# Kernel optimization log

Hardware: AMD Instinct MI355X
Metric: run time of the kernel (lower is better)

Reference implementation:

```python
import jax, jax.numpy as jnp
import numpy as np

N = 50000   # nodes
E = 600000  # edges
D = 128     # embedding_dim
L = 4       # num_message_passing_steps


def setup_inputs() -> dict:
    key = jax.random.key(0)
    ks = jax.random.split(key, 5)
    x = jax.random.normal(ks[0], (N, D), dtype=jnp.float32)
    edge_index = jax.random.randint(ks[1], (2, E), 0, N, dtype=jnp.int32)
    # Per-layer params: MPNN linear (no bias), GCNConv weight + bias.
    lin_w = jax.random.normal(ks[2], (L, D, D), dtype=jnp.float32) / np.sqrt(D).astype(np.float32)
    gcn_w = jax.random.normal(ks[3], (L, D, D), dtype=jnp.float32) / np.sqrt(D).astype(np.float32)
    gcn_b = jax.random.normal(ks[4], (L, D), dtype=jnp.float32) * 0.01
    return {"x": x, "edge_index": edge_index, "lin_w": lin_w, "gcn_w": gcn_w, "gcn_b": gcn_b}


def reference(x, edge_index, lin_w, gcn_w, gcn_b):
    n = x.shape[0]
    # GCNConv defaults: add_self_loops=True, normalize=True.
    loops = jnp.arange(n, dtype=edge_index.dtype)
    src = jnp.concatenate([edge_index[0], loops])  # [E+N]
    dst = jnp.concatenate([edge_index[1], loops])  # [E+N]
    # Degree computed on dst (col) for flow='source_to_target'.
    deg = jax.ops.segment_sum(jnp.ones_like(src, dtype=x.dtype), dst, num_segments=n)
    dinv = jnp.where(deg > 0, jax.lax.rsqrt(jnp.maximum(deg, 1.0)), 0.0)
    norm = dinv[src] * dinv[dst]  # [E+N]

    for l in range(lin_w.shape[0]):
        h = x @ lin_w[l].T                 # MPNNLayer.linear (no bias)
        h = h @ gcn_w[l].T                 # GCNConv internal linear
        msgs = h[src] * norm[:, None]      # gather + normalize  [E+N, D]
        agg = jax.ops.segment_sum(msgs, dst, num_segments=n)
        x = agg + gcn_b[l]                 # GCNConv bias
        # NOTE: self.relu is `Sequential as ReLU` -> empty Sequential = identity.
    return x
```

## Files before the change

kernel.cpp:

```cpp
#include <hip/hip_runtime.h>

#define DEMB 128

typedef __attribute__((ext_vector_type(8))) _Float16 half8;
typedef __attribute__((ext_vector_type(4))) _Float16 half4;
typedef __attribute__((ext_vector_type(4))) float f32x4;

__global__ void kwc(const float* __restrict__ gcn, const float* __restrict__ lin,
                    float* __restrict__ Ms) {
  __shared__ float sa[128];
  int l = blockIdx.x >> 7, i = blockIdx.x & 127, j = threadIdx.x;
  sa[j] = gcn[((size_t)l * 128 + i) * 128 + j];
  __syncthreads();
  float acc = 0.f;
#pragma unroll 8
  for (int k = 0; k < 128; ++k) acc += sa[k] * lin[((size_t)l * 128 + k) * 128 + j];
  Ms[((size_t)l * 128 + i) * 128 + j] = acc;
}

__global__ void ksg(const float* __restrict__ A, const float* __restrict__ B,
                    float* __restrict__ C) {
  __shared__ float sa[128];
  int i = blockIdx.x, j = threadIdx.x;
  sa[j] = A[i * 128 + j];
  __syncthreads();
  float acc = 0.f;
#pragma unroll 8
  for (int k = 0; k < 128; ++k) acc += sa[k] * B[k * 128 + j];
  C[i * 128 + j] = acc;
}

__global__ void ksgh(const float* __restrict__ A, const float* __restrict__ B,
                     _Float16* __restrict__ C) {
  __shared__ float sa[128];
  int i = blockIdx.x, j = threadIdx.x;
  sa[j] = A[i * 128 + j];
  __syncthreads();
  float acc = 0.f;
#pragma unroll 8
  for (int k = 0; k < 128; ++k) acc += sa[k] * B[k * 128 + j];
  C[i * 128 + j] = (_Float16)acc;
}

__global__ void kcvec(const float* __restrict__ Ms, const float* __restrict__ gb,
                      float* __restrict__ cb) {
  __shared__ float t0[128], t1[128];
  int j = threadIdx.x;
  const float* M1 = Ms + 16384;
  const float* M2 = Ms + 2 * 16384;
  const float* M3 = Ms + 3 * 16384;
  float a;
  t0[j] = gb[j]; __syncthreads();
  a = 0.f; for (int k = 0; k < 128; ++k) a += M1[j * 128 + k] * t0[k];
  t1[j] = a; __syncthreads();
  a = 0.f; for (int k = 0; k < 128; ++k) a += M2[j * 128 + k] * t1[k];
  __syncthreads(); t0[j] = a; __syncthreads();
  a = 0.f; for (int k = 0; k < 128; ++k) a += M3[j * 128 + k] * t0[k];
  cb[j] = a;
  __syncthreads(); t0[j] = gb[128 + j]; __syncthreads();
  a = 0.f; for (int k = 0; k < 128; ++k) a += M2[j * 128 + k] * t0[k];
  t1[j] = a; __syncthreads();
  a = 0.f; for (int k = 0; k < 128; ++k) a += M3[j * 128 + k] * t1[k];
  cb[128 + j] = a;
  __syncthreads(); t0[j] = gb[256 + j]; __syncthreads();
  a = 0.f; for (int k = 0; k < 128; ++k) a += M3[j * 128 + k] * t0[k];
  cb[256 + j] = a;
}

__global__ void kinit(int* __restrict__ deg, int* __restrict__ cur, int n) {
  int i = blockIdx.x * 256 + threadIdx.x;
  if (i < n) { deg[i] = 1; cur[i] = 0; }
}

__global__ void kdeg(const int* __restrict__ ei, int* __restrict__ deg, int etot) {
  int i = blockIdx.x * 256 + threadIdx.x;
  if (i < etot) atomicAdd(&deg[ei[etot + i]], 1);
}

__global__ void kscan1(const int* __restrict__ deg, int* __restrict__ off,
                       int* __restrict__ bsum, float* __restrict__ dinv,
                       float* __restrict__ dinv2, int n) {
  __shared__ int s[256];
  int t = threadIdx.x, i = blockIdx.x * 256 + t;
  int c = 0;
  if (i < n) {
    int d = deg[i];
    c = d - 1;
    float dv = rsqrtf((float)d);
    dinv[i] = dv;
    dinv2[i] = dv * dv;
  }
  s[t] = c;
  __syncthreads();
  for (int o = 1; o < 256; o <<= 1) {
    int v = (t >= o) ? s[t - o] : 0;
    __syncthreads();
    s[t] += v;
    __syncthreads();
  }
  if (i < n) off[i] = s[t] - c;
  if (t == 255) bsum[blockIdx.x] = s[t];
}

__global__ void kscan2(const int* __restrict__ bsum, int* __restrict__ boff,
                       int nb, int* __restrict__ off, int n, int etot) {
  __shared__ int s[256];
  int t = threadIdx.x;
  int c = (t < nb) ? bsum[t] : 0;
  s[t] = c;
  __syncthreads();
  for (int o = 1; o < 256; o <<= 1) {
    int v = (t >= o) ? s[t - o] : 0;
    __syncthreads();
    s[t] += v;
    __syncthreads();
  }
  if (t < nb) boff[t] = s[t] - c;
  if (t == 0) off[n] = etot;
}

__global__ void kscan3(int* __restrict__ off, const int* __restrict__ boff, int n) {
  int i = blockIdx.x * 256 + threadIdx.x;
  if (i < n) off[i] += boff[i >> 8];
}

__global__ void kfill(const int* __restrict__ ei, const int* __restrict__ off,
                      int* __restrict__ cur, int* __restrict__ csr, int etot) {
  int i = blockIdx.x * 256 + threadIdx.x;
  if (i < etot) {
    int d = ei[etot + i];
    int p = atomicAdd(&cur[d], 1);
    csr[off[d] + p] = ei[i];
  }
}

__global__ void kspmv(const float* __restrict__ a_in, const float* __restrict__ dinv,
                      const int* __restrict__ csr, const int* __restrict__ off,
                      float* __restrict__ u_out, float* __restrict__ a_out, int n) {
  int i = blockIdx.x * 256 + threadIdx.x;
  if (i >= n) return;
  float s = a_in[i];
  int e = off[i], end = off[i + 1];
  for (; e < end; ++e) s += a_in[csr[e]];
  float u = dinv[i] * s;
  u_out[i] = u;
  a_out[i] = dinv[i] * u;
}

__global__ void kpre(const float* __restrict__ x, const float* __restrict__ dinv,
                     _Float16* __restrict__ xh, int n) {
  int gid = blockIdx.x * 256 + threadIdx.x;
  if (gid >= n * 32) return;
  int r = gid >> 5, c = (gid & 31) * 4;
  float d = dinv[r];
  float4 v = *(const float4*)(x + (size_t)r * DEMB + c);
  half4 o = {(_Float16)(v.x * d), (_Float16)(v.y * d), (_Float16)(v.z * d), (_Float16)(v.w * d)};
  *(half4*)(xh + (size_t)r * DEMB + c) = o;
}

__launch_bounds__(256)
__global__ void kagg16(const _Float16* __restrict__ vin, const int* __restrict__ csr,
                       const int* __restrict__ off, const float* __restrict__ scale,
                       _Float16* __restrict__ vout, int n) {
  int wid = (int)((blockIdx.x * 256u + threadIdx.x) >> 6);
  if (wid >= n) return;
  int lane = threadIdx.x & 63;
  int q = lane >> 4, l16 = lane & 15;
  const _Float16* base = vin + (size_t)8 * l16;
  float acc[8];
  if (q == 0) {
    half8 sv = *(const half8*)(base + (size_t)wid * DEMB);
#pragma unroll
    for (int j = 0; j < 8; ++j) acc[j] = (float)sv[j];
  } else {
#pragma unroll
    for (int j = 0; j < 8; ++j) acc[j] = 0.f;
  }
  int end = off[wid + 1];
  for (int e = off[wid] + 4 * q; e < end; e += 16) {
    int em = end - 1;
    int i0 = csr[e];
    int i1 = csr[min(e + 1, em)];
    int i2 = csr[min(e + 2, em)];
    int i3 = csr[min(e + 3, em)];
    float w1 = (e + 1 < end) ? 1.f : 0.f;
    float w2 = (e + 2 < end) ? 1.f : 0.f;
    float w3 = (e + 3 < end) ? 1.f : 0.f;
    half8 r0 = *(const half8*)(base + (size_t)i0 * DEMB);
    half8 r1 = *(const half8*)(base + (size_t)i1 * DEMB);
    half8 r2 = *(const half8*)(base + (size_t)i2 * DEMB);
    half8 r3 = *(const half8*)(base + (size_t)i3 * DEMB);
#pragma unroll
    for (int j = 0; j < 8; ++j)
      acc[j] += (float)r0[j] + w1 * (float)r1[j] + w2 * (float)r2[j] + w3 * (float)r3[j];
  }
#pragma unroll
  for (int j = 0; j < 8; ++j) {
    acc[j] += __shfl_xor(acc[j], 16);
    acc[j] += __shfl_xor(acc[j], 32);
  }
  if (q == 0) {
    float s = scale[wid];
    half8 o;
#pragma unroll
    for (int j = 0; j < 8; ++j) o[j] = (_Float16)(acc[j] * s);
    *(half8*)(vout + (size_t)wid * DEMB + 8 * l16) = o;
  }
}

__launch_bounds__(256)
__global__ void kgemm16(const _Float16* __restrict__ y, const _Float16* __restrict__ Rh,
                        const float* __restrict__ u1, const float* __restrict__ u2,
                        const float* __restrict__ u3, const float* __restrict__ cb,
                        const float* __restrict__ b3, float* __restrict__ out, int n) {
  int t = threadIdx.x;
  int wv = t >> 6, lane = t & 63;
  int l16 = lane & 15, g = lane >> 4;
  int row0 = blockIdx.x * 128 + wv * 32;
  f32x4 acc[2][8];
#pragma unroll
  for (int w = 0; w < 2; ++w)
#pragma unroll
    for (int n8 = 0; n8 < 8; ++n8) acc[w][n8] = (f32x4){0.f, 0.f, 0.f, 0.f};

#pragma unroll
  for (int k0 = 0; k0 < 128; k0 += 32) {
    half8 a0 = *(const half8*)(y + (size_t)(row0 + l16) * DEMB + k0 + g * 8);
    half8 a1 = *(const half8*)(y + (size_t)(row0 + 16 + l16) * DEMB + k0 + g * 8);
#pragma unroll
    for (int n8 = 0; n8 < 8; ++n8) {
      half8 b = *(const half8*)(Rh + (size_t)(n8 * 16 + l16) * DEMB + k0 + g * 8);
      acc[0][n8] = __builtin_amdgcn_mfma_f32_16x16x32_f16(a0, b, acc[0][n8], 0, 0, 0);
      acc[1][n8] = __builtin_amdgcn_mfma_f32_16x16x32_f16(a1, b, acc[1][n8], 0, 0, 0);
    }
  }
#pragma unroll
  for (int n8 = 0; n8 < 8; ++n8) {
    int col = n8 * 16 + l16;
    float cA = cb[col], cB = cb[128 + col], cC = cb[256 + col], bb = b3[col];
#pragma unroll
    for (int w = 0; w < 2; ++w)
#pragma unroll
      for (int r = 0; r < 4; ++r) {
        int row = row0 + w * 16 + g * 4 + r;
        if (row < n) {
          out[(size_t)row * DEMB + col] =
              acc[w][n8][r] + u3[row] * cA + u2[row] * cB + u1[row] * cC + bb;
        }
      }
  }
}

extern "C" void kernel_launch(void* const* d_in, const int* in_sizes, int n_in,
                              void* d_out, int out_size, void* d_ws, size_t ws_size,
                              hipStream_t stream) {
  const float* x0 = (const float*)d_in[0];
  const int* ei = (const int*)d_in[1];
  const float* lin = (const float*)d_in[2];
  const float* gcn = (const float*)d_in[3];
  const float* gb = (const float*)d_in[4];
  float* out = (float*)d_out;

  int N = in_sizes[0] / DEMB;
  int E = in_sizes[1] / 2;
  int L = in_sizes[2] / (DEMB * DEMB);
  int NP = (N + 127) & ~127;

  char* w = (char*)d_ws;
  auto carve = [&](size_t bytes) {
    char* p = w;
    w += (bytes + 255) & ~(size_t)255;
    return p;
  };
  float* Ms    = (float*)carve((size_t)L * DEMB * DEMB * 4);
  float* A1    = (float*)carve((size_t)DEMB * DEMB * 4);
  float* A2    = (float*)carve((size_t)DEMB * DEMB * 4);
  _Float16* Rh = (_Float16*)carve((size_t)DEMB * DEMB * 2);
  float* cb    = (float*)carve((size_t)3 * DEMB * 4);
  float* dinv  = (float*)carve((size_t)N * 4);
  float* dnv2  = (float*)carve((size_t)N * 4);
  int* deg     = (int*)carve((size_t)N * 4);
  int* off     = (int*)carve((size_t)(N + 1) * 4);
  int* cur     = (int*)carve((size_t)N * 4);
  int* bsum    = (int*)carve(256 * 4);
  int* boff    = (int*)carve(256 * 4);
  int* csr     = (int*)carve((size_t)E * 4);
  float* u1    = (float*)carve((size_t)N * 4);
  float* u2    = (float*)carve((size_t)N * 4);
  float* u3    = (float*)carve((size_t)N * 4);
  float* a1    = (float*)carve((size_t)N * 4);
  _Float16* ha = (_Float16*)carve((size_t)NP * DEMB * 2);
  _Float16* hb = (_Float16*)carve((size_t)NP * DEMB * 2);
  float* a2    = (float*)cur;
  float* a3    = (float*)deg;
  (void)ws_size; (void)n_in; (void)out_size;

  int nbN = (N + 255) / 256;
  int nbE = (E + 255) / 256;

  kwc<<<L * DEMB, DEMB, 0, stream>>>(gcn, lin, Ms);
  ksg<<<DEMB, DEMB, 0, stream>>>(Ms + 16384, Ms, A1);
  ksg<<<DEMB, DEMB, 0, stream>>>(Ms + 2 * 16384, A1, A2);
  ksgh<<<DEMB, DEMB, 0, stream>>>(Ms + 3 * 16384, A2, Rh);
  kcvec<<<1, DEMB, 0, stream>>>(Ms, gb, cb);

  kinit<<<nbN, 256, 0, stream>>>(deg, cur, N);
  kdeg<<<nbE, 256, 0, stream>>>(ei, deg, E);
  kscan1<<<nbN, 256, 0, stream>>>(deg, off, bsum, dinv, dnv2, N);
  kscan2<<<1, 256, 0, stream>>>(bsum, boff, nbN, off, N, E);
  kscan3<<<nbN, 256, 0, stream>>>(off, boff, N);
  kfill<<<nbE, 256, 0, stream>>>(ei, off, cur, csr, E);

  kspmv<<<nbN, 256, 0, stream>>>(dinv, dinv, csr, off, u1, a1, N);
  kspmv<<<nbN, 256, 0, stream>>>(a1, dinv, csr, off, u2, a2, N);
  kspmv<<<nbN, 256, 0, stream>>>(a2, dinv, csr, off, u3, a3, N);

  kpre<<<(N * 32 + 255) / 256, 256, 0, stream>>>(x0, dinv, ha, N);
  kagg16<<<(N + 3) / 4, 256, 0, stream>>>(ha, csr, off, dnv2, hb, N);
  kagg16<<<(N + 3) / 4, 256, 0, stream>>>(hb, csr, off, dnv2, ha, N);
  kagg16<<<(N + 3) / 4, 256, 0, stream>>>(ha, csr, off, dnv2, hb, N);
  kagg16<<<(N + 3) / 4, 256, 0, stream>>>(hb, csr, off, dinv, ha, N);

  kgemm16<<<(N + 127) / 128, 256, 0, stream>>>(ha, Rh, u1, u2, u3, cb, gb + 3 * DEMB, out, N);
}
```

Before: 268.6 us.

## Fuse scalar SpMV into feature aggregation and restructure weight precompute

The three scalar SpMV passes are folded into the first three feature aggregation kernels through a template flag, which removes three launches and their extra CSR traversals. The aggregation now assigns 16 lanes per node instead of a 64-lane wave with a shuffle reduction, and unrolls the gather loop by 8 for more memory-level parallelism. The weight-matrix chain and bias-vector precompute are regrouped into two parallel kernels (associative reordering), and the CSR fill writes absolute positions so it no longer reads the offset array. The risk is load imbalance and lower occupancy per node for high-degree rows, and the fused kernels add a few extra scalar loads.

```diff
diff --git a/kernel.cpp b/kernel.cpp
--- a/kernel.cpp
+++ b/kernel.cpp
@@ -18,58 +18,79 @@
   Ms[((size_t)l * 128 + i) * 128 + j] = acc;
 }
 
-__global__ void ksg(const float* __restrict__ A, const float* __restrict__ B,
-                    float* __restrict__ C) {
-  __shared__ float sa[128];
-  int i = blockIdx.x, j = threadIdx.x;
-  sa[j] = A[i * 128 + j];
-  __syncthreads();
-  float acc = 0.f;
-#pragma unroll 8
-  for (int k = 0; k < 128; ++k) acc += sa[k] * B[k * 128 + j];
-  C[i * 128 + j] = acc;
-}
-
-__global__ void ksgh(const float* __restrict__ A, const float* __restrict__ B,
-                     _Float16* __restrict__ C) {
-  __shared__ float sa[128];
-  int i = blockIdx.x, j = threadIdx.x;
-  sa[j] = A[i * 128 + j];
-  __syncthreads();
-  float acc = 0.f;
-#pragma unroll 8
-  for (int k = 0; k < 128; ++k) acc += sa[k] * B[k * 128 + j];
-  C[i * 128 + j] = (_Float16)acc;
-}
-
-__global__ void kcvec(const float* __restrict__ Ms, const float* __restrict__ gb,
-                      float* __restrict__ cb) {
-  __shared__ float t0[128], t1[128];
-  int j = threadIdx.x;
+__global__ void kst2(const float* __restrict__ Ms, const float* __restrict__ gb,
+                     float* __restrict__ A1, float* __restrict__ B1,
+                     float* __restrict__ v0, float* __restrict__ cb) {
+  const float* M0 = Ms;
   const float* M1 = Ms + 16384;
   const float* M2 = Ms + 2 * 16384;
   const float* M3 = Ms + 3 * 16384;
-  float a;
-  t0[j] = gb[j]; __syncthreads();
-  a = 0.f; for (int k = 0; k < 128; ++k) a += M1[j * 128 + k] * t0[k];
-  t1[j] = a; __syncthreads();
-  a = 0.f; for (int k = 0; k < 128; ++k) a += M2[j * 128 + k] * t1[k];
-  __syncthreads(); t0[j] = a; __syncthreads();
-  a = 0.f; for (int k = 0; k < 128; ++k) a += M3[j * 128 + k] * t0[k];
-  cb[j] = a;
-  __syncthreads(); t0[j] = gb[128 + j]; __syncthreads();
-  a = 0.f; for (int k = 0; k < 128; ++k) a += M2[j * 128 + k] * t0[k];
-  t1[j] = a; __syncthreads();
-  a = 0.f; for (int k = 0; k < 128; ++k) a += M3[j * 128 + k] * t1[k];
-  cb[128 + j] = a;
-  __syncthreads(); t0[j] = gb[256 + j]; __syncthreads();
-  a = 0.f; for (int k = 0; k < 128; ++k) a += M3[j * 128 + k] * t0[k];
-  cb[256 + j] = a;
-}
-
-__global__ void kinit(int* __restrict__ deg, int* __restrict__ cur, int n) {
+  __shared__ float sa[128];
+  int b = blockIdx.x, j = threadIdx.x;
+  if (b < 128) {
+    sa[j] = M1[b * 128 + j];
+    __syncthreads();
+    float acc = 0.f;
+#pragma unroll 8
+    for (int k = 0; k < 128; ++k) acc += sa[k] * M0[k * 128 + j];
+    A1[b * 128 + j] = acc;
+  } else if (b < 256) {
+    int i = b - 128;
+    sa[j] = M3[i * 128 + j];
+    __syncthreads();
+    float acc = 0.f;
+#pragma unroll 8
+    for (int k = 0; k < 128; ++k) acc += sa[k] * M2[k * 128 + j];
+    B1[i * 128 + j] = acc;
+  } else if (b == 256) {
+    sa[j] = gb[j];
+    __syncthreads();
+    float acc = 0.f;
+#pragma unroll 8
+    for (int k = 0; k < 128; ++k) acc += M1[j * 128 + k] * sa[k];
+    v0[j] = acc;
+  } else {
+    sa[j] = gb[2 * 128 + j];
+    __syncthreads();
+    float acc = 0.f;
+#pragma unroll 8
+    for (int k = 0; k < 128; ++k) acc += M3[j * 128 + k] * sa[k];
+    cb[256 + j] = acc;
+  }
+}
+
+__global__ void kst3(const float* __restrict__ A1, const float* __restrict__ B1,
+                     const float* __restrict__ v0, const float* __restrict__ gb,
+                     _Float16* __restrict__ Rh, float* __restrict__ cb) {
+  __shared__ float sa[128];
+  int b = blockIdx.x, j = threadIdx.x;
+  if (b < 128) {
+    sa[j] = B1[b * 128 + j];
+    __syncthreads();
+    float acc = 0.f;
+#pragma unroll 8
+    for (int k = 0; k < 128; ++k) acc += sa[k] * A1[k * 128 + j];
+    Rh[b * 128 + j] = (_Float16)acc;
+  } else if (b == 128) {
+    sa[j] = v0[j];
+    __syncthreads();
+    float acc = 0.f;
+#pragma unroll 8
+    for (int k = 0; k < 128; ++k) acc += B1[j * 128 + k] * sa[k];
+    cb[j] = acc;
+  } else {
+    sa[j] = gb[128 + j];
+    __syncthreads();
+    float acc = 0.f;
+#pragma unroll 8
+    for (int k = 0; k < 128; ++k) acc += B1[j * 128 + k] * sa[k];
+    cb[128 + j] = acc;
+  }
+}
+
+__global__ void kinit(int* __restrict__ deg, int n) {
   int i = blockIdx.x * 256 + threadIdx.x;
-  if (i < n) { deg[i] = 1; cur[i] = 0; }
+  if (i < n) deg[i] = 0;
 }
 
 __global__ void kdeg(const int* __restrict__ ei, int* __restrict__ deg, int etot) {
@@ -84,9 +105,8 @@
   int t = threadIdx.x, i = blockIdx.x * 256 + t;
   int c = 0;
   if (i < n) {
-    int d = deg[i];
-    c = d - 1;
-    float dv = rsqrtf((float)d);
+    c = deg[i];
+    float dv = rsqrtf((float)(c + 1));
     dinv[i] = dv;
     dinv2[i] = dv * dv;
   }
@@ -119,32 +139,24 @@
   if (t == 0) off[n] = etot;
 }
 
-__global__ void kscan3(int* __restrict__ off, const int* __restrict__ boff, int n) {
+__global__ void kscan3(int* __restrict__ off, const int* __restrict__ boff,
+                       int* __restrict__ cur, int n) {
   int i = blockIdx.x * 256 + threadIdx.x;
-  if (i < n) off[i] += boff[i >> 8];
-}
-
-__global__ void kfill(const int* __restrict__ ei, const int* __restrict__ off,
-                      int* __restrict__ cur, int* __restrict__ csr, int etot) {
+  if (i < n) {
+    int o = off[i] + boff[i >> 8];
+    off[i] = o;
+    cur[i] = o;
+  }
+}
+
+__global__ void kfill(const int* __restrict__ ei, int* __restrict__ cur,
+                      int* __restrict__ csr, int etot) {
   int i = blockIdx.x * 256 + threadIdx.x;
   if (i < etot) {
     int d = ei[etot + i];
     int p = atomicAdd(&cur[d], 1);
-    csr[off[d] + p] = ei[i];
-  }
-}
-
-__global__ void kspmv(const float* __restrict__ a_in, const float* __restrict__ dinv,
-                      const int* __restrict__ csr, const int* __restrict__ off,
-                      float* __restrict__ u_out, float* __restrict__ a_out, int n) {
-  int i = blockIdx.x * 256 + threadIdx.x;
-  if (i >= n) return;
-  float s = a_in[i];
-  int e = off[i], end = off[i + 1];
-  for (; e < end; ++e) s += a_in[csr[e]];
-  float u = dinv[i] * s;
-  u_out[i] = u;
-  a_out[i] = dinv[i] * u;
+    csr[p] = ei[i];
+  }
 }
 
 __global__ void kpre(const float* __restrict__ x, const float* __restrict__ dinv,
@@ -158,53 +170,78 @@
   *(half4*)(xh + (size_t)r * DEMB + c) = o;
 }
 
+template <int WITHU>
 __launch_bounds__(256)
 __global__ void kagg16(const _Float16* __restrict__ vin, const int* __restrict__ csr,
                        const int* __restrict__ off, const float* __restrict__ scale,
+                       const float* __restrict__ dinv, const float* __restrict__ a_in,
+                       float* __restrict__ u_out, float* __restrict__ a_out,
                        _Float16* __restrict__ vout, int n) {
-  int wid = (int)((blockIdx.x * 256u + threadIdx.x) >> 6);
-  if (wid >= n) return;
-  int lane = threadIdx.x & 63;
-  int q = lane >> 4, l16 = lane & 15;
-  const _Float16* base = vin + (size_t)8 * l16;
+  int node = (int)((blockIdx.x * 256u + threadIdx.x) >> 4);
+  if (node >= n) return;
+  int l16 = threadIdx.x & 15;
+  const _Float16* base = vin + 8 * l16;
+  half8 sv = *(const half8*)(base + (size_t)node * DEMB);
   float acc[8];
-  if (q == 0) {
-    half8 sv = *(const half8*)(base + (size_t)wid * DEMB);
-#pragma unroll
-    for (int j = 0; j < 8; ++j) acc[j] = (float)sv[j];
-  } else {
-#pragma unroll
-    for (int j = 0; j < 8; ++j) acc[j] = 0.f;
-  }
-  int end = off[wid + 1];
-  for (int e = off[wid] + 4 * q; e < end; e += 16) {
+#pragma unroll
+  for (int j = 0; j < 8; ++j) acc[j] = (float)sv[j];
+  float s = WITHU ? a_in[node] : 0.f;
+  int e = off[node], end = off[node + 1];
+  for (; e + 8 <= end; e += 8) {
+    int i0 = csr[e], i1 = csr[e + 1], i2 = csr[e + 2], i3 = csr[e + 3];
+    int i4 = csr[e + 4], i5 = csr[e + 5], i6 = csr[e + 6], i7 = csr[e + 7];
+    half8 r0 = *(const half8*)(base + (size_t)i0 * DEMB);
+    half8 r1 = *(const half8*)(base + (size_t)i1 * DEMB);
+    half8 r2 = *(const half8*)(base + (size_t)i2 * DEMB);
+    half8 r3 = *(const half8*)(base + (size_t)i3 * DEMB);
+    half8 r4 = *(const half8*)(base + (size_t)i4 * DEMB);
+    half8 r5 = *(const half8*)(base + (size_t)i5 * DEMB);
+    half8 r6 = *(const half8*)(base + (size_t)i6 * DEMB);
+    half8 r7 = *(const half8*)(base + (size_t)i7 * DEMB);
+    if (WITHU)
+      s += a_in[i0] + a_in[i1] + a_in[i2] + a_in[i3] +
+           a_in[i4] + a_in[i5] + a_in[i6] + a_in[i7];
+#pragma unroll
+    for (int j = 0; j < 8; ++j)
+      acc[j] += ((float)r0[j] + (float)r1[j]) + ((float)r2[j] + (float)r3[j]) +
+                ((float)r4[j] + (float)r5[j]) + ((float)r6[j] + (float)r7[j]);
+  }
+  for (; e + 4 <= end; e += 4) {
+    int i0 = csr[e], i1 = csr[e + 1], i2 = csr[e + 2], i3 = csr[e + 3];
+    half8 r0 = *(const half8*)(base + (size_t)i0 * DEMB);
+    half8 r1 = *(const half8*)(base + (size_t)i1 * DEMB);
+    half8 r2 = *(const half8*)(base + (size_t)i2 * DEMB);
+    half8 r3 = *(const half8*)(base + (size_t)i3 * DEMB);
+    if (WITHU) s += a_in[i0] + a_in[i1] + a_in[i2] + a_in[i3];
+#pragma unroll
+    for (int j = 0; j < 8; ++j)
+      acc[j] += ((float)r0[j] + (float)r1[j]) + ((float)r2[j] + (float)r3[j]);
+  }
+  if (e < end) {
     int em = end - 1;
     int i0 = csr[e];
     int i1 = csr[min(e + 1, em)];
     int i2 = csr[min(e + 2, em)];
-    int i3 = csr[min(e + 3, em)];
     float w1 = (e + 1 < end) ? 1.f : 0.f;
     float w2 = (e + 2 < end) ? 1.f : 0.f;
-    float w3 = (e + 3 < end) ? 1.f : 0.f;
     half8 r0 = *(const half8*)(base + (size_t)i0 * DEMB);
     half8 r1 = *(const half8*)(base + (size_t)i1 * DEMB);
     half8 r2 = *(const half8*)(base + (size_t)i2 * DEMB);
-    half8 r3 = *(const half8*)(base + (size_t)i3 * DEMB);
+    if (WITHU) s += a_in[i0] + w1 * a_in[i1] + w2 * a_in[i2];
 #pragma unroll
     for (int j = 0; j < 8; ++j)
-      acc[j] += (float)r0[j] + w1 * (float)r1[j] + w2 * (float)r2[j] + w3 * (float)r3[j];
-  }
-#pragma unroll
-  for (int j = 0; j < 8; ++j) {
-    acc[j] += __shfl_xor(acc[j], 16);
-    acc[j] += __shfl_xor(acc[j], 32);
-  }
-  if (q == 0) {
-    float s = scale[wid];
-    half8 o;
-#pragma unroll
-    for (int j = 0; j < 8; ++j) o[j] = (_Float16)(acc[j] * s);
-    *(half8*)(vout + (size_t)wid * DEMB + 8 * l16) = o;
+      acc[j] += (float)r0[j] + w1 * (float)r1[j] + w2 * (float)r2[j];
+  }
+  float sc = scale[node];
+  half8 o;
+#pragma unroll
+  for (int j = 0; j < 8; ++j) o[j] = (_Float16)(acc[j] * sc);
+  *(half8*)(vout + (size_t)node * DEMB + 8 * l16) = o;
+  if (WITHU && l16 == 0) {
+    float dv = dinv[node];
+    float u = dv * s;
+    u_out[node] = u;
+    a_out[node] = dv * u;
   }
 }
 
@@ -274,8 +311,9 @@
   };
   float* Ms    = (float*)carve((size_t)L * DEMB * DEMB * 4);
   float* A1    = (float*)carve((size_t)DEMB * DEMB * 4);
-  float* A2    = (float*)carve((size_t)DEMB * DEMB * 4);
+  float* B1    = (float*)carve((size_t)DEMB * DEMB * 4);
   _Float16* Rh = (_Float16*)carve((size_t)DEMB * DEMB * 2);
+  float* v0    = (float*)carve((size_t)DEMB * 4);
   float* cb    = (float*)carve((size_t)3 * DEMB * 4);
   float* dinv  = (float*)carve((size_t)N * 4);
   float* dnv2  = (float*)carve((size_t)N * 4);
@@ -289,37 +327,32 @@
   float* u2    = (float*)carve((size_t)N * 4);
   float* u3    = (float*)carve((size_t)N * 4);
   float* a1    = (float*)carve((size_t)N * 4);
+  float* a2    = (float*)carve((size_t)N * 4);
+  float* a3    = (float*)carve((size_t)N * 4);
   _Float16* ha = (_Float16*)carve((size_t)NP * DEMB * 2);
   _Float16* hb = (_Float16*)carve((size_t)NP * DEMB * 2);
-  float* a2    = (float*)cur;
-  float* a3    = (float*)deg;
   (void)ws_size; (void)n_in; (void)out_size;
 
   int nbN = (N + 255) / 256;
   int nbE = (E + 255) / 256;
+  int nbA = (N * 16 + 255) / 256;
 
   kwc<<<L * DEMB, DEMB, 0, stream>>>(gcn, lin, Ms);
-  ksg<<<DEMB, DEMB, 0, stream>>>(Ms + 16384, Ms, A1);
-  ksg<<<DEMB, DEMB, 0, stream>>>(Ms + 2 * 16384, A1, A2);
-  ksgh<<<DEMB, DEMB, 0, stream>>>(Ms + 3 * 16384, A2, Rh);
-  kcvec<<<1, DEMB, 0, stream>>>(Ms, gb, cb);
-
-  kinit<<<nbN, 256, 0, stream>>>(deg, cur, N);
+  kst2<<<258, DEMB, 0, stream>>>(Ms, gb, A1, B1, v0, cb);
+  kst3<<<130, DEMB, 0, stream>>>(A1, B1, v0, gb, Rh, cb);
+
+  kinit<<<nbN, 256, 0, stream>>>(deg, N);
   kdeg<<<nbE, 256, 0, stream>>>(ei, deg, E);
   kscan1<<<nbN, 256, 0, stream>>>(deg, off, bsum, dinv, dnv2, N);
   kscan2<<<1, 256, 0, stream>>>(bsum, boff, nbN, off, N, E);
-  kscan3<<<nbN, 256, 0, stream>>>(off, boff, N);
-  kfill<<<nbE, 256, 0, stream>>>(ei, off, cur, csr, E);
-
-  kspmv<<<nbN, 256, 0, stream>>>(dinv, dinv, csr, off, u1, a1, N);
-  kspmv<<<nbN, 256, 0, stream>>>(a1, dinv, csr, off, u2, a2, N);
-  kspmv<<<nbN, 256, 0, stream>>>(a2, dinv, csr, off, u3, a3, N);
+  kscan3<<<nbN, 256, 0, stream>>>(off, boff, cur, N);
+  kfill<<<nbE, 256, 0, stream>>>(ei, cur, csr, E);
 
   kpre<<<(N * 32 + 255) / 256, 256, 0, stream>>>(x0, dinv, ha, N);
-  kagg16<<<(N + 3) / 4, 256, 0, stream>>>(ha, csr, off, dnv2, hb, N);
-  kagg16<<<(N + 3) / 4, 256, 0, stream>>>(hb, csr, off, dnv2, ha, N);
-  kagg16<<<(N + 3) / 4, 256, 0, stream>>>(ha, csr, off, dnv2, hb, N);
-  kagg16<<<(N + 3) / 4, 256, 0, stream>>>(hb, csr, off, dinv, ha, N);
+  kagg16<1><<<nbA, 256, 0, stream>>>(ha, csr, off, dnv2, dinv, dinv, u1, a1, hb, N);
+  kagg16<1><<<nbA, 256, 0, stream>>>(hb, csr, off, dnv2, dinv, a1, u2, a2, ha, N);
+  kagg16<1><<<nbA, 256, 0, stream>>>(ha, csr, off, dnv2, dinv, a2, u3, a3, hb, N);
+  kagg16<0><<<nbA, 256, 0, stream>>>(hb, csr, off, dinv, dinv, nullptr, nullptr, nullptr, ha, N);
 
   kgemm16<<<(N + 127) / 128, 256, 0, stream>>>(ha, Rh, u1, u2, u3, cb, gb + 3 * DEMB, out, N);
 }
```

Measured after the change: 221.8 us. -17.4%, faster.
